# Performance work log

Measured on AMD Instinct MI355X. Metric: run time of the kernel, lower is better.

The kernel has to match this reference:

```python
import jax, jax.numpy as jnp
import numpy as np

V, D, H, F, L, M, T, B, MAXT = 32000, 1024, 16, 4096, 3, 1, 1024, 2, 2048
HD = D // H

def _ln(x, g, b, eps=1e-5):
    m = x.mean(-1, keepdims=True)
    v = ((x - m) ** 2).mean(-1, keepdims=True)
    return (x - m) * jax.lax.rsqrt(v + eps) * g + b

def _mha(x, Wq, bq, Wk, bk, Wv, bv, Wo, bo, mask):
    Bx, Tx, Dx = x.shape
    q = (x @ Wq.T + bq).reshape(Bx, Tx, H, HD)
    k = (x @ Wk.T + bk).reshape(Bx, Tx, H, HD)
    v = (x @ Wv.T + bv).reshape(Bx, Tx, H, HD)
    s = jnp.einsum('bqhd,bkhd->bhqk', q, k) / np.float32(np.sqrt(HD))
    s = jnp.where(mask[None, None], s, jnp.float32(-1e9))
    a = jax.nn.softmax(s, axis=-1)
    o = jnp.einsum('bhqk,bkhd->bqhd', a, v).reshape(Bx, Tx, Dx)
    return o @ Wo.T + bo

def setup_inputs() -> dict:
    key = jax.random.key(0)
    ks = iter(jax.random.split(key, 64))
    rn = lambda shape: jax.random.normal(next(ks), shape, jnp.float32) * 0.02
    inp = {
        'x': jax.random.randint(next(ks), (B, T), 0, V),
        'mask': jnp.tril(jnp.ones((T, T), bool)),  # causal mask
        'tok_W': rn((V, D)),  # embedding table = Linear(V,D).weight.T
        'pos_embed': rn((MAXT, D)),
        'Wq': rn((L, D, D)), 'bq': jnp.zeros((L, D)),
        'Wk': rn((L, D, D)), 'bk': jnp.zeros((L, D)),
        'Wv': rn((L, D, D)), 'bv': jnp.zeros((L, D)),
        'Wo': rn((L, D, D)), 'bo': jnp.zeros((L, D)),
        'ln1_g': jnp.ones((L, D)), 'ln1_b': jnp.zeros((L, D)),
        'W1': rn((L, F, D)), 'b1': jnp.zeros((L, F)),
        'W2': rn((L, D, F)), 'b2': jnp.zeros((L, D)),
        'ln2_g': jnp.ones((L, D)), 'ln2_b': jnp.zeros((L, D)),
        'mWq': rn((M, D, D)), 'mbq': jnp.zeros((M, D)),
        'mWk': rn((M, D, D)), 'mbk': jnp.zeros((M, D)),
        'mWv': rn((M, D, D)), 'mbv': jnp.zeros((M, D)),
        'mWo': rn((M, D, D)), 'mbo': jnp.zeros((M, D)),
        'mln_g': jnp.ones((M, D)), 'mln_b': jnp.zeros((M, D)),
        'tWq': rn((D, D)), 'tbq': jnp.zeros((D,)),
        'tWk': rn((D, D)), 'tbk': jnp.zeros((D,)),
        'tWv': rn((D, D)), 'tbv': jnp.zeros((D,)),
        'tWo': rn((D, D)), 'tbo': jnp.zeros((D,)),
        'tln_g': jnp.ones((D,)), 'tln_b': jnp.zeros((D,)),
        'norm_g': jnp.ones((D,)), 'norm_b': jnp.zeros((D,)),
        'out_W': rn((V, D)), 'out_b': jnp.zeros((V,)),
    }
    return inp

def reference(x, mask, tok_W, pos_embed, Wq, bq, Wk, bk, Wv, bv, Wo, bo,
              ln1_g, ln1_b, W1, b1, W2, b2, ln2_g, ln2_b,
              mWq, mbq, mWk, mbk, mWv, mbv, mWo, mbo, mln_g, mln_b,
              tWq, tbq, tWk, tbk, tWv, tbv, tWo, tbo, tln_g, tln_b,
              norm_g, norm_b, out_W, out_b):
    Bx, Tx = x.shape
    # one_hot(x, V).float() @ W_tok^T  ==  gather row x from the (V, D) table
    h = jnp.take(tok_W, x, axis=0) + pos_embed[:Tx][None]
    mi = 0
    for i in range(L):  # static small layer count
        a = _mha(h, Wq[i], bq[i], Wk[i], bk[i], Wv[i], bv[i], Wo[i], bo[i], mask)
        h = _ln(h + a, ln1_g[i], ln1_b[i])
        f = jax.nn.gelu(h @ W1[i].T + b1[i]) @ W2[i].T + b2[i]
        h = _ln(h + f, ln2_g[i], ln2_b[i])
        if i % 3 == 2 and mi < M:  # memory layer every 3rd block
            a = _mha(h, mWq[mi], mbq[mi], mWk[mi], mbk[mi], mWv[mi], mbv[mi], mWo[mi], mbo[mi], mask)
            h = _ln(h + a, mln_g[mi], mln_b[mi])
            mi += 1
    a = _mha(h, tWq, tbq, tWk, tbk, tWv, tbv, tWo, tbo, mask)  # thought attention
    h = _ln(h + a, tln_g, tln_b)
    h = _ln(h, norm_g, norm_b)
    return h @ out_W.T + out_b  # [B, T, V] logits
```

## Files before the change

kernel.cpp:

```cpp
#include <hip/hip_runtime.h>
#include <cstdint>

#define DEV static __device__ __forceinline__

typedef unsigned short u16;
typedef __attribute__((ext_vector_type(8))) short short8;
typedef __attribute__((ext_vector_type(4))) float f32x4;

namespace cfg {
constexpr int V = 32000, D = 1024, H = 16, F = 4096, L = 3, T = 1024, B = 2;
constexpr int N = B * T;
constexpr int HD = D / H;
}

DEV float bf2f(u16 b) { union { unsigned u; float f; } x; x.u = (unsigned)b << 16; return x.f; }
DEV u16 f2bf(float f) {
  union { float f; unsigned u; } x; x.f = f;
  unsigned u = x.u;
  return (u16)((u + 0x7fffu + ((u >> 16) & 1u)) >> 16);
}

DEV void gload16(void* lds, const void* g) {
  __builtin_amdgcn_global_load_lds((__attribute__((address_space(1))) void*)g,
                                   (__attribute__((address_space(3))) void*)lds, 16, 0, 0);
}

template <int NW>
DEV void waitVm() {
  if constexpr (NW == 0) asm volatile("s_waitcnt vmcnt(0)" ::: "memory");
  else if constexpr (NW == 4) asm volatile("s_waitcnt vmcnt(4)" ::: "memory");
  else if constexpr (NW == 8) asm volatile("s_waitcnt vmcnt(8)" ::: "memory");
  __builtin_amdgcn_sched_barrier(0);
}
DEV void barrierRaw() {
  __builtin_amdgcn_sched_barrier(0);
  __builtin_amdgcn_s_barrier();
  __builtin_amdgcn_sched_barrier(0);
}
DEV void waitLgkm0() {
  asm volatile("s_waitcnt lgkmcnt(0)" ::: "memory");
  __builtin_amdgcn_sched_barrier(0);
}

DEV float waveSum(float v) {
#pragma unroll
  for (int o = 32; o; o >>= 1) v += __shfl_xor(v, o);
  return v;
}

struct CastJob { const float* src; u16* dst; int nBlk; };
struct CastArgs { CastJob j[24]; int n; };

__global__ void cast_kernel(CastArgs a) {
  int blk = blockIdx.x;
  int i = 0;
  while (i + 1 < a.n && blk >= a.j[i].nBlk) { blk -= a.j[i].nBlk; ++i; }
  const size_t base = (size_t)blk * 2048 + threadIdx.x * 8;
  const float4* s4 = (const float4*)(a.j[i].src + base);
  const float4 v0 = s4[0], v1 = s4[1];
  short8 o;
  o[0] = (short)f2bf(v0.x); o[1] = (short)f2bf(v0.y);
  o[2] = (short)f2bf(v0.z); o[3] = (short)f2bf(v0.w);
  o[4] = (short)f2bf(v1.x); o[5] = (short)f2bf(v1.y);
  o[6] = (short)f2bf(v1.z); o[7] = (short)f2bf(v1.w);
  *(short8*)(a.j[i].dst + base) = o;
}

struct CopyJob { const float* src; float* dst; };
struct CopyArgs { CopyJob j[16]; int n; };
__global__ void bconcat_kernel(CopyArgs a) {
  const CopyJob jb = a.j[blockIdx.x];
  ((float4*)jb.dst)[threadIdx.x] = ((const float4*)jb.src)[threadIdx.x];
}

__global__ void embed_kernel(const int* __restrict__ x, const float* __restrict__ tokW,
                             const float* __restrict__ pos, float* __restrict__ hF,
                             u16* __restrict__ hB) {
  const int bt = blockIdx.x;
  const int t = bt & (cfg::T - 1);
  const int tid = threadIdx.x;
  const int idx = x[bt];
  float4 v = ((const float4*)(tokW + (size_t)idx * cfg::D))[tid];
  const float4 p = ((const float4*)(pos + (size_t)t * cfg::D))[tid];
  v.x += p.x; v.y += p.y; v.z += p.z; v.w += p.w;
  ((float4*)(hF + (size_t)bt * cfg::D))[tid] = v;
  union { u16 u[4]; uint2 q; } pk;
  pk.u[0] = f2bf(v.x); pk.u[1] = f2bf(v.y); pk.u[2] = f2bf(v.z); pk.u[3] = f2bf(v.w);
  *(uint2*)(hB + (size_t)bt * cfg::D + tid * 4) = pk.q;
}

template <int NADD>
__global__ void ln_kernel(const float* __restrict__ base,
                          const float* __restrict__ a0, const float* __restrict__ a1,
                          const float* __restrict__ a2, const float* __restrict__ a3,
                          const float* __restrict__ biasv,
                          const float* __restrict__ g, const float* __restrict__ bt,
                          float* __restrict__ outF, u16* __restrict__ outB) {
  const int row = blockIdx.x, tid = threadIdx.x;
  const int lane = tid & 63, wid = tid >> 6;
  const size_t roff = (size_t)row * cfg::D;
  float4 x = ((const float4*)(base + roff))[tid];
  if (NADD >= 1) {
    const float4 a = ((const float4*)(a0 + roff))[tid];
    x.x += a.x; x.y += a.y; x.z += a.z; x.w += a.w;
  }
  if (NADD >= 2) {
    const float4 a = ((const float4*)(a1 + roff))[tid];
    x.x += a.x; x.y += a.y; x.z += a.z; x.w += a.w;
  }
  if (NADD >= 3) {
    const float4 a = ((const float4*)(a2 + roff))[tid];
    x.x += a.x; x.y += a.y; x.z += a.z; x.w += a.w;
  }
  if (NADD >= 4) {
    const float4 a = ((const float4*)(a3 + roff))[tid];
    x.x += a.x; x.y += a.y; x.z += a.z; x.w += a.w;
  }
  if (biasv) {
    const float4 a = ((const float4*)biasv)[tid];
    x.x += a.x; x.y += a.y; x.z += a.z; x.w += a.w;
  }
  float s = x.x + x.y + x.z + x.w;
  float s2 = x.x * x.x + x.y * x.y + x.z * x.z + x.w * x.w;
  __shared__ float sb[8];
  s = waveSum(s); s2 = waveSum(s2);
  if (lane == 0) { sb[wid] = s; sb[4 + wid] = s2; }
  __syncthreads();
  s = sb[0] + sb[1] + sb[2] + sb[3];
  s2 = sb[4] + sb[5] + sb[6] + sb[7];
  const float mean = s * (1.f / cfg::D);
  const float rs = rsqrtf(s2 * (1.f / cfg::D) - mean * mean + 1e-5f);
  const float4 gv = ((const float4*)g)[tid];
  const float4 bv = ((const float4*)bt)[tid];
  float4 y;
  y.x = (x.x - mean) * rs * gv.x + bv.x;
  y.y = (x.y - mean) * rs * gv.y + bv.y;
  y.z = (x.z - mean) * rs * gv.z + bv.z;
  y.w = (x.w - mean) * rs * gv.w + bv.w;
  ((float4*)(outF + roff))[tid] = y;
  union { u16 u[4]; uint2 q; } pk;
  pk.u[0] = f2bf(y.x); pk.u[1] = f2bf(y.y); pk.u[2] = f2bf(y.z); pk.u[3] = f2bf(y.w);
  *(uint2*)(outB + roff + tid * 4) = pk.q;
}

__global__ void vtrans_kernel(const u16* __restrict__ v, u16* __restrict__ vtO, int vstride) {
  __shared__ u16 s[64][68];
  const int bh = blockIdx.y, b = bh >> 4, h = bh & 15;
  const int t0 = blockIdx.x * 64;
  const int tid = threadIdx.x;
  const int r2 = tid >> 3, cg = tid & 7;
#pragma unroll
  for (int p = 0; p < 2; ++p) {
    const int r = p * 32 + r2;
    const short8 val = *(const short8*)(v + (size_t)(b * cfg::T + t0 + r) * vstride + h * 64 + cg * 8);
#pragma unroll
    for (int j = 0; j < 8; ++j) s[r][cg * 8 + j] = (u16)val[j];
  }
  __syncthreads();
#pragma unroll
  for (int p = 0; p < 2; ++p) {
    const int d = p * 32 + r2;
    short8 o;
#pragma unroll
    for (int j = 0; j < 8; ++j) o[j] = (short)s[cg * 8 + j][d];
    *(short8*)(vtO + ((size_t)bh * 64 + d) * (size_t)cfg::T + t0 + cg * 8) = o;
  }
}

template <int NCH>
DEV void stageTile(u16* lds, const u16* src, int strideElems, int tid) {
#pragma unroll
  for (int c = 0; c < NCH / 256; ++c) {
    const int ci = c * 256 + tid;
    const int r = ci >> 3;
    const int c8 = ci & 7;
    const int sc8 = c8 ^ (r & 7);
    gload16(lds + (size_t)ci * 8, src + (size_t)r * strideElems + sc8 * 8);
  }
}
DEV short8 ldsFrag(const u16* tile, int row, int kElem) {
  const int byteoff = row * 128 + ((kElem * 2) ^ ((row & 7) << 4));
  return *(const short8*)((const char*)tile + byteoff);
}
DEV short8 ldsFrag32(const u16* tile, int row, int kElem) {
  const int byteoff = row * 64 + ((kElem * 2) ^ (((row >> 1) & 3) << 4));
  return *(const short8*)((const char*)tile + byteoff);
}

__launch_bounds__(256, 3)
__global__ void fattn_kernel(const u16* __restrict__ qkv, const u16* __restrict__ vt,
                             u16* __restrict__ o) {
  constexpr int D3 = 3 * cfg::D;
  __shared__ u16 Qs[64 * 64];
  __shared__ u16 Ks[64 * 64];
  __shared__ u16 Vs[64 * 64];
  __shared__ u16 Ps[64][72];
  const int tid = threadIdx.x, lane = tid & 63, w = tid >> 6;
  const int qt = gridDim.x - 1 - blockIdx.x;
  const int bh = blockIdx.y;
  const int b = bh >> 4, h = bh & 15;
  const int q0 = qt * 64;
  const int l15 = lane & 15, lq = lane >> 4;

  stageTile<512>(Qs, qkv + (size_t)(b * cfg::T + q0) * D3 + h * 64, D3, tid);
  __syncthreads();
  short8 qf[2];
#pragma unroll
  for (int kk = 0; kk < 2; ++kk)
    qf[kk] = ldsFrag(Qs, w * 16 + l15, kk * 32 + lq * 8);

  f32x4 oa[4];
  float m[4], l[4];
#pragma unroll
  for (int r = 0; r < 4; ++r) { m[r] = -1e30f; l[r] = 0.f; }
#pragma unroll
  for (int nt = 0; nt < 4; ++nt) { oa[nt][0] = 0; oa[nt][1] = 0; oa[nt][2] = 0; oa[nt][3] = 0; }

  const int nkt = qt + 1;
  const u16* kbase = qkv + (size_t)(b * cfg::T) * D3 + cfg::D + h * 64;
  const u16* vbase = vt + (size_t)bh * 64 * cfg::T;

  for (int kt = 0; kt < nkt; ++kt) {
    const int k0 = kt * 64;
    __syncthreads();
    stageTile<512>(Ks, kbase + (size_t)k0 * D3, D3, tid);
    stageTile<512>(Vs, vbase + k0, cfg::T, tid);
    __syncthreads();

    f32x4 sa[4];
#pragma unroll
    for (int nt = 0; nt < 4; ++nt) { sa[nt][0] = 0; sa[nt][1] = 0; sa[nt][2] = 0; sa[nt][3] = 0; }
#pragma unroll
    for (int kk = 0; kk < 2; ++kk) {
      short8 kf[4];
#pragma unroll
      for (int nt = 0; nt < 4; ++nt) kf[nt] = ldsFrag(Ks, nt * 16 + l15, kk * 32 + lq * 8);
#pragma unroll
      for (int nt = 0; nt < 4; ++nt)
        sa[nt] = __builtin_amdgcn_mfma_f32_16x16x32_bf16(qf[kk], kf[nt], sa[nt], 0, 0, 0);
    }

    const bool needMask = (kt >= qt);
#pragma unroll
    for (int r = 0; r < 4; ++r) {
      const int qrow = q0 + w * 16 + lq * 4 + r;
      float s[4];
#pragma unroll
      for (int nt = 0; nt < 4; ++nt) {
        s[nt] = sa[nt][r] * 0.125f;
        if (needMask && (k0 + nt * 16 + l15 > qrow)) s[nt] = -3e38f;
      }
      float rm = fmaxf(fmaxf(s[0], s[1]), fmaxf(s[2], s[3]));
#pragma unroll
      for (int off = 1; off < 16; off <<= 1) rm = fmaxf(rm, __shfl_xor(rm, off));
      const float mn = fmaxf(m[r], rm);
      const float sc = __expf(m[r] - mn);
      m[r] = mn;
      float ps = 0.f;
#pragma unroll
      for (int nt = 0; nt < 4; ++nt) {
        const float p = __expf(s[nt] - mn);
        ps += p;
        Ps[w * 16 + lq * 4 + r][nt * 16 + l15] = f2bf(p);
      }
#pragma unroll
      for (int off = 1; off < 16; off <<= 1) ps += __shfl_xor(ps, off);
      l[r] = l[r] * sc + ps;
#pragma unroll
      for (int nt = 0; nt < 4; ++nt) oa[nt][r] *= sc;
    }

#pragma unroll
    for (int kk = 0; kk < 2; ++kk) {
      short8 pa = *(const short8*)&Ps[w * 16 + l15][kk * 32 + lq * 8];
      short8 vf[4];
#pragma unroll
      for (int nt = 0; nt < 4; ++nt) vf[nt] = ldsFrag(Vs, nt * 16 + l15, kk * 32 + lq * 8);
#pragma unroll
      for (int nt = 0; nt < 4; ++nt)
        oa[nt] = __builtin_amdgcn_mfma_f32_16x16x32_bf16(pa, vf[nt], oa[nt], 0, 0, 0);
    }
  }

  u16* obase = o + (size_t)(b * cfg::T + q0 + w * 16) * cfg::D + h * 64;
#pragma unroll
  for (int r = 0; r < 4; ++r) {
    const float inv = 1.f / l[r];
    const int rl = lq * 4 + r;
#pragma unroll
    for (int nt = 0; nt < 4; ++nt)
      obase[(size_t)rl * cfg::D + nt * 16 + l15] = f2bf(oa[nt][r] * inv);
  }
}

template <int BN, int EPI, int OUTF32, int SWZ, int MMAJOR>
__launch_bounds__(256, 4)
__global__ void gemm_kernel(const u16* __restrict__ A, const u16* __restrict__ Bw,
                            const float* __restrict__ bias, void* __restrict__ Cp,
                            int lda, int ldb, int ldc, int K, long long partStride) {
  constexpr int BM = 128, BK = 64;
  constexpr int WN = BN / 2;
  constexpr int MF = 4, NF = WN / 16;
  int bx = blockIdx.x, by = blockIdx.y;
  if (SWZ) {
    const int gx = gridDim.x;
    const int nwg = gx * gridDim.y;
    const int lid = by * gx + bx;
    const int q = nwg >> 3, r = nwg & 7;
    const int xcd = lid & 7, rest = lid >> 3;
    const int nid = (xcd < r ? xcd * (q + 1) : r * (q + 1) + (xcd - r) * q) + rest;
    bx = nid % gx; by = nid / gx;
  }
  const int z = blockIdx.z;
  const u16* Ab = A + (size_t)z * K;
  const u16* Bb = Bw + (size_t)z * K;
  const int tid = threadIdx.x;
  const int lane = tid & 63;
  const int wid = tid >> 6;
  const int wr = wid >> 1, wc = wid & 1;
  const int m0 = (MMAJOR ? bx : by) * BM;
  const int n0 = (MMAJOR ? by : bx) * BN;

  __shared__ u16 As[BM][BK];
  __shared__ u16 Bs[BN][BK];

  const int nkt = K / BK;

  f32x4 acc[MF][NF];
#pragma unroll
  for (int i = 0; i < MF; ++i)
#pragma unroll
    for (int j = 0; j < NF; ++j) {
      acc[i][j][0] = 0.f; acc[i][j][1] = 0.f; acc[i][j][2] = 0.f; acc[i][j][3] = 0.f;
    }

  for (int kt = 0; kt < nkt; ++kt) {
    __syncthreads();
    const int kb = kt * BK;
    stageTile<(BM * BK) / 8>(&As[0][0], Ab + (size_t)m0 * lda + kb, lda, tid);
    stageTile<(BN * BK) / 8>(&Bs[0][0], Bb + (size_t)n0 * ldb + kb, ldb, tid);
    __syncthreads();
#pragma unroll
    for (int kk = 0; kk < BK / 32; ++kk) {
      short8 av[MF], bv[NF];
      const int kElem = kk * 32 + (lane >> 4) * 8;
#pragma unroll
      for (int mt = 0; mt < MF; ++mt)
        av[mt] = ldsFrag(&As[0][0], wr * 64 + mt * 16 + (lane & 15), kElem);
#pragma unroll
      for (int nt = 0; nt < NF; ++nt)
        bv[nt] = ldsFrag(&Bs[0][0], wc * WN + nt * 16 + (lane & 15), kElem);
#pragma unroll
      for (int mt = 0; mt < MF; ++mt)
#pragma unroll
        for (int nt = 0; nt < NF; ++nt)
          acc[mt][nt] = __builtin_amdgcn_mfma_f32_16x16x32_bf16(av[mt], bv[nt], acc[mt][nt], 0, 0, 0);
    }
  }

  const int rhi = (lane >> 4) * 4, cidx = lane & 15;
  const long long cb = (long long)z * partStride;
#pragma unroll
  for (int mt = 0; mt < MF; ++mt) {
#pragma unroll
    for (int nt = 0; nt < NF; ++nt) {
      const int col = n0 + wc * WN + nt * 16 + cidx;
      const float badd = bias ? bias[col] : 0.f;
#pragma unroll
      for (int r = 0; r < 4; ++r) {
        const int row = m0 + wr * 64 + mt * 16 + rhi + r;
        float val = acc[mt][nt][r] + badd;
        if (EPI == 1) {
          const float zz = 1.5957691216057308f * (val + 0.044715f * val * val * val);
          const float th = 1.f - 2.f / (__expf(zz) + 1.f);
          val = 0.5f * val * (1.f + th);
        }
        const size_t off = (size_t)(cb + (long long)row * ldc + col);
        if (OUTF32) ((float*)Cp)[off] = val;
        else ((u16*)Cp)[off] = f2bf(val);
      }
    }
  }
}

__launch_bounds__(512, 1)
__global__ void gemm256c_kernel(const u16* __restrict__ A, const u16* __restrict__ Bw,
                                const float* __restrict__ bias, float* __restrict__ Cp,
                                int lda, int ldb, int ldc, int K) {
  extern __shared__ u16 lds[];
  int bx = blockIdx.x, by = blockIdx.y;
  {
    const int gx = gridDim.x;
    const int nwg = gx * gridDim.y;
    const int lid = by * gx + bx;
    const int q = nwg >> 3, r = nwg & 7;
    const int xcd = lid & 7, rest = lid >> 3;
    const int nid = (xcd < r ? xcd * (q + 1) : r * (q + 1) + (xcd - r) * q) + rest;
    bx = nid % gx; by = nid / gx;
  }
  const int tid = threadIdx.x;
  const int lane = tid & 63;
  const int wid = tid >> 6;
  const int wr = wid >> 2, wc = wid & 3;
  const int m0 = bx * 256;
  const int n0 = by * 256;
  const int l15 = lane & 15, lq = lane >> 4;

  const u16* Abase = A + (size_t)m0 * lda;
  const u16* Bbase = Bw + (size_t)n0 * ldb;

  auto stageHalf = [&](int ldsOff, const u16* srcBase, int ld, int kb, int h) {
    const int ci = h * 512 + tid;
    const int r = ci >> 2;
    const int sc = (ci & 3) ^ ((r >> 1) & 3);
    gload16(lds + ldsOff + (size_t)ci * 8, srcBase + (size_t)r * ld + kb + sc * 8);
  };
  auto stageA = [&](int buf, int kb) {
    stageHalf(buf * 16384, Abase, lda, kb, 0);
    stageHalf(buf * 16384, Abase, lda, kb, 1);
  };
  auto stageB = [&](int buf, int kb) {
    stageHalf(buf * 16384 + 8192, Bbase, ldb, kb, 0);
    stageHalf(buf * 16384 + 8192, Bbase, ldb, kb, 1);
  };

  f32x4 acc[8][4];
#pragma unroll
  for (int i = 0; i < 8; ++i)
#pragma unroll
    for (int j = 0; j < 4; ++j) { acc[i][j][0] = 0.f; acc[i][j][1] = 0.f; acc[i][j][2] = 0.f; acc[i][j][3] = 0.f; }

  const int nt_ = K / 32;
  for (int t = 0; t < 3; ++t) { stageA(t, t * 32); stageB(t, t * 32); }

  const int kE = lq * 8;
  for (int t = 0; t < nt_; ++t) {
    if (t <= nt_ - 3) waitVm<8>();
    else if (t == nt_ - 2) waitVm<4>();
    else waitVm<0>();
    barrierRaw();
    const int buf = t & 3;
    const u16* At = lds + buf * 16384;
    const u16* Bt = lds + buf * 16384 + 8192;
    const int nbuf = (t + 3) & 3;
    const int kb3 = (t + 3) * 32;
    const bool pf = (t + 3 < nt_);
#pragma unroll
    for (int mh = 0; mh < 2; ++mh) {
      short8 av[4], bv[4];
#pragma unroll
      for (int mt = 0; mt < 4; ++mt)
        av[mt] = ldsFrag32(At, wr * 128 + mh * 64 + mt * 16 + l15, kE);
#pragma unroll
      for (int nt = 0; nt < 4; ++nt)
        bv[nt] = ldsFrag32(Bt, wc * 64 + nt * 16 + l15, kE);
      if (pf) {
        if (mh == 0) stageA(nbuf, kb3);
        else stageB(nbuf, kb3);
      }
      waitLgkm0();
      __builtin_amdgcn_s_setprio(1);
#pragma unroll
      for (int mt = 0; mt < 4; ++mt)
#pragma unroll
        for (int nt = 0; nt < 4; ++nt)
          acc[mh * 4 + mt][nt] = __builtin_amdgcn_mfma_f32_16x16x32_bf16(av[mt], bv[nt], acc[mh * 4 + mt][nt], 0, 0, 0);
      __builtin_amdgcn_s_setprio(0);
    }
  }

#pragma unroll
  for (int g = 0; g < 8; ++g) {
#pragma unroll
    for (int nt = 0; nt < 4; ++nt) {
      const int col = n0 + wc * 64 + nt * 16 + l15;
      const float badd = bias[col];
#pragma unroll
      for (int r = 0; r < 4; ++r) {
        const int row = m0 + wr * 128 + g * 16 + lq * 4 + r;
        Cp[(size_t)row * ldc + col] = acc[g][nt][r] + badd;
      }
    }
  }
}

extern "C" void kernel_launch(void* const* d_in, const int* in_sizes, int n_in,
                              void* d_out, int out_size, void* d_ws, size_t ws_size,
                              hipStream_t stream) {
  using namespace cfg;
  (void)in_sizes; (void)n_in; (void)out_size;
  const int* x = (const int*)d_in[0];
  const float* tokW = (const float*)d_in[2];
  const float* pos = (const float*)d_in[3];
  const float* Wq = (const float*)d_in[4];  const float* bq = (const float*)d_in[5];
  const float* Wk = (const float*)d_in[6];  const float* bk = (const float*)d_in[7];
  const float* Wv = (const float*)d_in[8];  const float* bv = (const float*)d_in[9];
  const float* Wo = (const float*)d_in[10]; const float* bo = (const float*)d_in[11];
  const float* ln1g = (const float*)d_in[12]; const float* ln1b = (const float*)d_in[13];
  const float* W1 = (const float*)d_in[14]; const float* b1 = (const float*)d_in[15];
  const float* W2 = (const float*)d_in[16]; const float* b2 = (const float*)d_in[17];
  const float* ln2g = (const float*)d_in[18]; const float* ln2b = (const float*)d_in[19];
  const float* mWq = (const float*)d_in[20]; const float* mbq = (const float*)d_in[21];
  const float* mWk = (const float*)d_in[22]; const float* mbk = (const float*)d_in[23];
  const float* mWv = (const float*)d_in[24]; const float* mbv = (const float*)d_in[25];
  const float* mWo = (const float*)d_in[26]; const float* mbo = (const float*)d_in[27];
  const float* mlng = (const float*)d_in[28]; const float* mlnb = (const float*)d_in[29];
  const float* tWq = (const float*)d_in[30]; const float* tbq = (const float*)d_in[31];
  const float* tWk = (const float*)d_in[32]; const float* tbk = (const float*)d_in[33];
  const float* tWv = (const float*)d_in[34]; const float* tbv = (const float*)d_in[35];
  const float* tWo = (const float*)d_in[36]; const float* tbo = (const float*)d_in[37];
  const float* tlng = (const float*)d_in[38]; const float* tlnb = (const float*)d_in[39];
  const float* normg = (const float*)d_in[40]; const float* normb = (const float*)d_in[41];
  const float* outW = (const float*)d_in[42]; const float* outb = (const float*)d_in[43];

  const size_t DD = (size_t)D * D;
  const long long ND = (long long)N * D;
  char* wsb = (char*)d_ws;
  size_t off = 0;
  auto alloc = [&](size_t bytes) {
    void* p = wsb + off;
    off += (bytes + 255) & ~(size_t)255;
    return p;
  };
  u16* qkvW = (u16*)alloc((size_t)L * 3 * DD * 2);
  u16* mqkvW = (u16*)alloc(3 * DD * 2);
  u16* tqkvW = (u16*)alloc(3 * DD * 2);
  u16* WoB = (u16*)alloc((size_t)L * DD * 2);
  u16* W1B = (u16*)alloc((size_t)L * F * D * 2);
  u16* W2B = (u16*)alloc((size_t)L * D * F * 2);
  u16* mWoB = (u16*)alloc(DD * 2);
  u16* tWoB = (u16*)alloc(DD * 2);
  u16* outWB = (u16*)alloc((size_t)V * D * 2);
  float* biasQKV = (float*)alloc((size_t)(L + 2) * 3 * D * 4);
  float* hF = (float*)alloc((size_t)N * D * 4);
  u16* hB = (u16*)alloc((size_t)N * D * 2);
  float* pS = (float*)alloc((size_t)4 * N * D * 4);
  u16* qkvB = (u16*)alloc((size_t)N * 3 * D * 2);
  u16* vtB = (u16*)alloc((size_t)N * D * 2);
  u16* oB = (u16*)alloc((size_t)N * D * 2);
  u16* f1B = (u16*)alloc((size_t)N * F * 2);
  if (off > ws_size) return;

  CastArgs ca;
  int nj = 0; long total = 0;
  auto addJob = [&](const float* s, u16* dptr, size_t n) {
    ca.j[nj].src = s; ca.j[nj].dst = dptr; ca.j[nj].nBlk = (int)(n / 2048);
    total += (long)(n / 2048); ++nj;
  };
  for (int i = 0; i < L; ++i) {
    addJob(Wq + i * DD, qkvW + (size_t)i * 3 * DD, DD);
    addJob(Wk + i * DD, qkvW + (size_t)i * 3 * DD + DD, DD);
    addJob(Wv + i * DD, qkvW + (size_t)i * 3 * DD + 2 * DD, DD);
  }
  addJob(mWq, mqkvW, DD); addJob(mWk, mqkvW + DD, DD); addJob(mWv, mqkvW + 2 * DD, DD);
  addJob(tWq, tqkvW, DD); addJob(tWk, tqkvW + DD, DD); addJob(tWv, tqkvW + 2 * DD, DD);
  addJob(Wo, WoB, (size_t)L * DD);
  addJob(W1, W1B, (size_t)L * F * D);
  addJob(W2, W2B, (size_t)L * D * F);
  addJob(mWo, mWoB, DD); addJob(tWo, tWoB, DD);
  addJob(outW, outWB, (size_t)V * D);
  ca.n = nj;
  cast_kernel<<<dim3((unsigned)total), 256, 0, stream>>>(ca);

  CopyArgs cpa;
  int nc = 0;
  auto addCopy = [&](const float* s, float* dptr) { cpa.j[nc].src = s; cpa.j[nc].dst = dptr; ++nc; };
  for (int i = 0; i < L; ++i) {
    addCopy(bq + (size_t)i * D, biasQKV + (size_t)i * 3 * D);
    addCopy(bk + (size_t)i * D, biasQKV + (size_t)i * 3 * D + D);
    addCopy(bv + (size_t)i * D, biasQKV + (size_t)i * 3 * D + 2 * D);
  }
  addCopy(mbq, biasQKV + (size_t)L * 3 * D); addCopy(mbk, biasQKV + (size_t)L * 3 * D + D);
  addCopy(mbv, biasQKV + (size_t)L * 3 * D + 2 * D);
  addCopy(tbq, biasQKV + (size_t)(L + 1) * 3 * D); addCopy(tbk, biasQKV + (size_t)(L + 1) * 3 * D + D);
  addCopy(tbv, biasQKV + (size_t)(L + 1) * 3 * D + 2 * D);
  cpa.n = nc;
  bconcat_kernel<<<dim3((unsigned)nc), 256, 0, stream>>>(cpa);

  embed_kernel<<<N, 256, 0, stream>>>(x, tokW, pos, hF, hB);

  auto mha = [&](const u16* qkvw, const float* qkvbias, const u16* wo) {
    gemm_kernel<64, 0, 0, 0, 0><<<dim3(3 * D / 64, N / 128, 1), 256, 0, stream>>>(
        hB, qkvw, qkvbias, qkvB, D, D, 3 * D, D, 0);
    vtrans_kernel<<<dim3(T / 64, B * H), 256, 0, stream>>>(qkvB + 2 * D, vtB, 3 * D);
    fattn_kernel<<<dim3(T / 64, B * H), 256, 0, stream>>>(qkvB, vtB, oB);
    gemm_kernel<64, 0, 1, 0, 0><<<dim3(D / 64, N / 128, 4), 256, 0, stream>>>(
        oB, wo, nullptr, pS, D, D, D, 256, ND);
  };
  auto lnMha = [&](const float* obias, const float* g, const float* b_) {
    ln_kernel<4><<<N, 256, 0, stream>>>(hF, pS, pS + ND, pS + 2 * ND, pS + 3 * ND,
                                        obias, g, b_, hF, hB);
  };

  int mi = 0;
  for (int i = 0; i < L; ++i) {
    mha(qkvW + (size_t)i * 3 * DD, biasQKV + (size_t)i * 3 * D, WoB + (size_t)i * DD);
    lnMha(bo + (size_t)i * D, ln1g + (size_t)i * D, ln1b + (size_t)i * D);
    gemm_kernel<64, 1, 0, 0, 0><<<dim3(F / 64, N / 128, 1), 256, 0, stream>>>(
        hB, W1B + (size_t)i * F * D, b1 + (size_t)i * F, f1B, D, D, F, D, 0);
    gemm_kernel<64, 0, 1, 0, 0><<<dim3(D / 64, N / 128, 4), 256, 0, stream>>>(
        f1B, W2B + (size_t)i * D * F, nullptr, pS, F, F, D, 1024, ND);
    ln_kernel<4><<<N, 256, 0, stream>>>(hF, pS, pS + ND, pS + 2 * ND, pS + 3 * ND,
                                        b2 + (size_t)i * D, ln2g + (size_t)i * D,
                                        ln2b + (size_t)i * D, hF, hB);
    if (i % 3 == 2 && mi < 1) {
      mha(mqkvW, biasQKV + (size_t)L * 3 * D, mWoB);
      lnMha(mbo, mlng, mlnb);
      ++mi;
    }
  }
  mha(tqkvW, biasQKV + (size_t)(L + 1) * 3 * D, tWoB);
  lnMha(tbo, tlng, tlnb);
  ln_kernel<0><<<N, 256, 0, stream>>>(hF, nullptr, nullptr, nullptr, nullptr, nullptr,
                                      normg, normb, hF, hB);

  hipError_t e = hipFuncSetAttribute(
      reinterpret_cast<const void*>(gemm256c_kernel),
      hipFuncAttributeMaxDynamicSharedMemorySize, 131072);
  if (e == hipSuccess) {
    gemm256c_kernel<<<dim3(N / 256, V / 256, 1), 512, 131072, stream>>>(
        hB, outWB, outb, (float*)d_out, D, D, V, D);
  } else {
    gemm_kernel<128, 0, 1, 1, 1><<<dim3(N / 128, V / 128, 1), 256, 0, stream>>>(
        hB, outWB, outb, (float*)d_out, D, D, V, D, 0);
  }
}
```

Measured before the change: 906.0 us.

## Add 4-stage pipelined direct-to-LDS GEMM for QKV and FFN-up projections

Adds a new 128x64-tile GEMM kernel that loads A and B straight into LDS through global_load_lds, keeps three k-steps of prefetch in flight across four buffers, and uses XOR-swizzled LDS placement. It replaces the generic gemm_kernel for the QKV projection and the first FFN GEMM (with fused GELU). The goal is to hide global-load latency behind the MFMA work and run three blocks per CU. Separately, the large 256-tile logits GEMM now loads its B fragments once per k-step instead of once per M half. Costs are more kernel code, extra register pressure from holding the B fragments longer, and a fixed swizzle pattern that ties the kernel to these tile shapes.

```diff
diff --git a/kernel.cpp b/kernel.cpp
--- a/kernel.cpp
+++ b/kernel.cpp
@@ -28,7 +28,9 @@
 template <int NW>
 DEV void waitVm() {
   if constexpr (NW == 0) asm volatile("s_waitcnt vmcnt(0)" ::: "memory");
+  else if constexpr (NW == 3) asm volatile("s_waitcnt vmcnt(3)" ::: "memory");
   else if constexpr (NW == 4) asm volatile("s_waitcnt vmcnt(4)" ::: "memory");
+  else if constexpr (NW == 6) asm volatile("s_waitcnt vmcnt(6)" ::: "memory");
   else if constexpr (NW == 8) asm volatile("s_waitcnt vmcnt(8)" ::: "memory");
   __builtin_amdgcn_sched_barrier(0);
 }
@@ -383,6 +385,96 @@
   }
 }
 
+template <int EPI>
+__launch_bounds__(256, 3)
+__global__ void gemmdp_kernel(const u16* __restrict__ A, const u16* __restrict__ Bw,
+                              const float* __restrict__ bias, u16* __restrict__ Cp,
+                              int lda, int ldb, int ldc, int K) {
+  __shared__ u16 lds[4 * 6144];
+  const int tid = threadIdx.x;
+  const int lane = tid & 63;
+  const int wid = tid >> 6;
+  const int wr = wid >> 1, wc = wid & 1;
+  const int m0 = blockIdx.y * 128;
+  const int n0 = blockIdx.x * 64;
+  const int l15 = lane & 15, lq = lane >> 4;
+
+  const u16* Abase = A + (size_t)m0 * lda;
+  const u16* Bbase = Bw + (size_t)n0 * ldb;
+
+  auto stage = [&](int buf, int kb) {
+#pragma unroll
+    for (int c = 0; c < 2; ++c) {
+      const int ci = c * 256 + tid;
+      const int r = ci >> 2;
+      const int sc = (ci & 3) ^ ((r >> 1) & 3);
+      gload16(lds + buf * 6144 + (size_t)ci * 8, Abase + (size_t)r * lda + kb + sc * 8);
+    }
+    {
+      const int ci = tid;
+      const int r = ci >> 2;
+      const int sc = (ci & 3) ^ ((r >> 1) & 3);
+      gload16(lds + buf * 6144 + 4096 + (size_t)ci * 8, Bbase + (size_t)r * ldb + kb + sc * 8);
+    }
+  };
+
+  f32x4 acc[4][2];
+#pragma unroll
+  for (int i = 0; i < 4; ++i)
+#pragma unroll
+    for (int j = 0; j < 2; ++j) { acc[i][j][0] = 0.f; acc[i][j][1] = 0.f; acc[i][j][2] = 0.f; acc[i][j][3] = 0.f; }
+
+  const int nt_ = K / 32;
+  for (int t = 0; t < 3; ++t) stage(t, t * 32);
+
+  const int kE = lq * 8;
+  for (int t = 0; t < nt_; ++t) {
+    if (t < nt_ - 2) waitVm<6>();
+    else if (t == nt_ - 2) waitVm<3>();
+    else waitVm<0>();
+    barrierRaw();
+    const int buf = t & 3;
+    const u16* At = lds + buf * 6144;
+    const u16* Bt = lds + buf * 6144 + 4096;
+    short8 av[4], bv[2];
+#pragma unroll
+    for (int mt = 0; mt < 4; ++mt)
+      av[mt] = ldsFrag32(At, wr * 64 + mt * 16 + l15, kE);
+#pragma unroll
+    for (int nt = 0; nt < 2; ++nt)
+      bv[nt] = ldsFrag32(Bt, wc * 32 + nt * 16 + l15, kE);
+    if (t + 3 < nt_) stage((t + 3) & 3, (t + 3) * 32);
+    waitLgkm0();
+    __builtin_amdgcn_s_setprio(1);
+#pragma unroll
+    for (int mt = 0; mt < 4; ++mt)
+#pragma unroll
+      for (int nt = 0; nt < 2; ++nt)
+        acc[mt][nt] = __builtin_amdgcn_mfma_f32_16x16x32_bf16(av[mt], bv[nt], acc[mt][nt], 0, 0, 0);
+    __builtin_amdgcn_s_setprio(0);
+  }
+
+#pragma unroll
+  for (int mt = 0; mt < 4; ++mt) {
+#pragma unroll
+    for (int nt = 0; nt < 2; ++nt) {
+      const int col = n0 + wc * 32 + nt * 16 + l15;
+      const float badd = bias[col];
+#pragma unroll
+      for (int r = 0; r < 4; ++r) {
+        const int row = m0 + wr * 64 + mt * 16 + lq * 4 + r;
+        float val = acc[mt][nt][r] + badd;
+        if (EPI == 1) {
+          const float zz = 1.5957691216057308f * (val + 0.044715f * val * val * val);
+          const float th = 1.f - 2.f / (__expf(zz) + 1.f);
+          val = 0.5f * val * (1.f + th);
+        }
+        Cp[(size_t)row * ldc + col] = f2bf(val);
+      }
+    }
+  }
+}
+
 __launch_bounds__(512, 1)
 __global__ void gemm256c_kernel(const u16* __restrict__ A, const u16* __restrict__ Bw,
                                 const float* __restrict__ bias, float* __restrict__ Cp,
@@ -445,15 +537,16 @@
     const int nbuf = (t + 3) & 3;
     const int kb3 = (t + 3) * 32;
     const bool pf = (t + 3 < nt_);
+    short8 bv[4];
+#pragma unroll
+    for (int nt = 0; nt < 4; ++nt)
+      bv[nt] = ldsFrag32(Bt, wc * 64 + nt * 16 + l15, kE);
 #pragma unroll
     for (int mh = 0; mh < 2; ++mh) {
-      short8 av[4], bv[4];
+      short8 av[4];
 #pragma unroll
       for (int mt = 0; mt < 4; ++mt)
         av[mt] = ldsFrag32(At, wr * 128 + mh * 64 + mt * 16 + l15, kE);
-#pragma unroll
-      for (int nt = 0; nt < 4; ++nt)
-        bv[nt] = ldsFrag32(Bt, wc * 64 + nt * 16 + l15, kE);
       if (pf) {
         if (mh == 0) stageA(nbuf, kb3);
         else stageB(nbuf, kb3);
@@ -580,8 +673,8 @@
   embed_kernel<<<N, 256, 0, stream>>>(x, tokW, pos, hF, hB);
 
   auto mha = [&](const u16* qkvw, const float* qkvbias, const u16* wo) {
-    gemm_kernel<64, 0, 0, 0, 0><<<dim3(3 * D / 64, N / 128, 1), 256, 0, stream>>>(
-        hB, qkvw, qkvbias, qkvB, D, D, 3 * D, D, 0);
+    gemmdp_kernel<0><<<dim3(3 * D / 64, N / 128, 1), 256, 0, stream>>>(
+        hB, qkvw, qkvbias, qkvB, D, D, 3 * D, D);
     vtrans_kernel<<<dim3(T / 64, B * H), 256, 0, stream>>>(qkvB + 2 * D, vtB, 3 * D);
     fattn_kernel<<<dim3(T / 64, B * H), 256, 0, stream>>>(qkvB, vtB, oB);
     gemm_kernel<64, 0, 1, 0, 0><<<dim3(D / 64, N / 128, 4), 256, 0, stream>>>(
@@ -596,8 +689,8 @@
   for (int i = 0; i < L; ++i) {
     mha(qkvW + (size_t)i * 3 * DD, biasQKV + (size_t)i * 3 * D, WoB + (size_t)i * DD);
     lnMha(bo + (size_t)i * D, ln1g + (size_t)i * D, ln1b + (size_t)i * D);
-    gemm_kernel<64, 1, 0, 0, 0><<<dim3(F / 64, N / 128, 1), 256, 0, stream>>>(
-        hB, W1B + (size_t)i * F * D, b1 + (size_t)i * F, f1B, D, D, F, D, 0);
+    gemmdp_kernel<1><<<dim3(F / 64, N / 128, 1), 256, 0, stream>>>(
+        hB, W1B + (size_t)i * F * D, b1 + (size_t)i * F, f1B, D, D, F, D);
     gemm_kernel<64, 0, 1, 0, 0><<<dim3(D / 64, N / 128, 4), 256, 0, stream>>>(
         f1B, W2B + (size_t)i * D * F, nullptr, pS, F, F, D, 1024, ND);
     ln_kernel<4><<<N, 256, 0, stream>>>(hF, pS, pS + ND, pS + 2 * ND, pS + 3 * ND,
```

Result: slower. 932.0 us (+2.9%).
